# Performance work log

Measured on AMD Instinct MI355X. Metric: run time of the kernel, lower is better.

The kernel has to match this reference:

```python
import jax, jax.numpy as jnp
import numpy as np

TEMPERATURE = 0.1  # init kwarg
EPS = 1e-8        # torch cosine_similarity eps


def setup_inputs() -> dict:
    key = jax.random.key(0)
    k1, k2, k3 = jax.random.split(key, 3)
    B, D, C = 4096, 1024, 32
    representations = jax.random.normal(k1, (B, D), dtype=jnp.float32)
    soft_labels = jax.random.uniform(k2, (B, C), dtype=jnp.float32)
    labels = jax.random.randint(k3, (B,), 0, 32, dtype=jnp.int64)
    return {
        "representations": representations,
        "soft_labels": soft_labels,
        "labels": labels,
        "pseudo_weight": 10,
    }


def reference(representations, soft_labels, labels, pseudo_weight):
    B = representations.shape[0]
    # row-normalize (cosine similarity)
    norms = jnp.maximum(jnp.linalg.norm(representations, axis=1, keepdims=True), EPS)
    rn = representations / norms
    Z = (rn @ rn.T) / TEMPERATURE                      # [B, B] scaled cosine sims
    E = jnp.exp(Z)
    off_diag = 1.0 - jnp.eye(B, dtype=Z.dtype)         # exclude j == i
    denom = jnp.sum(E * off_diag, axis=1, keepdims=True)   # [B, 1]
    loss_arr = -(Z - jnp.log(denom))                   # -log(exp(Z_ij)/denom_i)
    # positive-pair weights: same label, j != i (detached in original)
    pos = (labels[:, None] == labels[None, :]).astype(Z.dtype) * off_diag
    soft_sim = jax.lax.stop_gradient(soft_labels @ soft_labels.T)  # torch.inner, detached
    w = pos + pseudo_weight * soft_sim
    return jnp.sum(loss_arr * w) / B
```

## Files before the change

### kernel.cpp

```cpp
#include <hip/hip_runtime.h>
#include <hip/hip_bf16.h>
#include <stdint.h>


typedef float f32x4 __attribute__((ext_vector_type(4)));
typedef long i64;

#define INV_T 10.0f
#define Z_SCALE (INV_T / 256.0f)

#define GLD16(gp, lp)                                                          \
    __builtin_amdgcn_global_load_lds(                                          \
        (const __attribute__((address_space(1))) uint32_t*)(gp),               \
        (__attribute__((address_space(3))) uint32_t*)(lp), 16, 0, 0)

#define OFF_RNF8  0
#define OFF_DENOM 4194304
#define OFF_POSS  (OFF_DENOM + 16384)
#define OFF_G     (OFF_POSS + 16384)
#define OFF_OACC  (OFF_G + 131072)
#define OFF_DONE  (OFF_OACC + 16)
#define ZERO_SPAN 167936
#define OFF_CSP   (OFF_DENOM + ZERO_SPAN)
#define OFF_CCP   (OFF_CSP + 4096)
#define OFF_W     (OFF_CCP + 4096)

__global__ __launch_bounds__(256) void scl_stage1(const float* __restrict__ rep,
                                                  const float* __restrict__ sl,
                                                  const int* __restrict__ labels,
                                                  uint32_t* __restrict__ rnf8,
                                                  float* __restrict__ cs_part,
                                                  int* __restrict__ cc_part,
                                                  char* __restrict__ zbase) {
    int b = blockIdx.x;
    int t = threadIdx.x;
    if (b < 4096) {
        int row = b;
        const float4* src = reinterpret_cast<const float4*>(rep + (size_t)row * 1024);
        float4 v = src[t];
        float s = v.x * v.x + v.y * v.y + v.z * v.z + v.w * v.w;
#pragma unroll
        for (int m = 1; m < 64; m <<= 1) s += __shfl_xor(s, m, 64);
        __shared__ float red[4];
        if ((t & 63) == 0) red[t >> 6] = s;
        __syncthreads();
        s = red[0] + red[1] + red[2] + red[3];
        float nf = 16.0f / fmaxf(sqrtf(s), 1e-8f);
        int p = 0;
        p = __builtin_amdgcn_cvt_pk_fp8_f32(v.x * nf, v.y * nf, p, false);
        p = __builtin_amdgcn_cvt_pk_fp8_f32(v.z * nf, v.w * nf, p, true);
        rnf8[row * 256 + t] = (uint32_t)p;
    } else if (b < 4128) {
        __shared__ float part[8][32];
        __shared__ int bins[32];
        int bb = b - 4096;
        if (t < 32) bins[t] = 0;
        __syncthreads();
        if (t < 128) atomicAdd(&bins[labels[bb * 128 + t]], 1);
        int c = t & 31, rg = t >> 5;
        float s = 0.f;
#pragma unroll 4
        for (int k = 0; k < 16; ++k) {
            int i = bb * 128 + rg * 16 + k;
            s += sl[i * 32 + c];
        }
        part[rg][c] = s;
        __syncthreads();
        if (t < 32) {
            float tot = 0.f;
#pragma unroll
            for (int g = 0; g < 8; ++g) tot += part[g][t];
            cs_part[bb * 32 + t] = tot;
            cc_part[bb * 32 + t] = bins[t];
        }
    } else {
        int zb = b - 4128;
        *(uint4*)(zbase + (size_t)zb * 4096 + t * 16) = (uint4){0, 0, 0, 0};
    }
}

__global__ __launch_bounds__(256) void scl_main(const uint8_t* __restrict__ rnf8,
                                                const float* __restrict__ sl,
                                                const int* __restrict__ labels,
                                                const float* __restrict__ cs_part,
                                                const int* __restrict__ cc_part,
                                                const int* __restrict__ pwp,
                                                float* __restrict__ denom,
                                                float* __restrict__ posS,
                                                float* __restrict__ G,
                                                float* __restrict__ W) {
    int tid = threadIdx.x;

    if (blockIdx.x >= 528) {
        if (blockIdx.x < 1040) {
            int idx = blockIdx.x - 528;
            int dblk = idx & 15, ks = idx >> 4;
            int dq = tid >> 5, c = tid & 31;
            int d0 = dblk * 64 + dq * 8;
            float acc[8];
#pragma unroll
            for (int j = 0; j < 8; ++j) acc[j] = 0.f;
            int i0 = ks * 128;
#pragma unroll 4
            for (int k = 0; k < 128; ++k) {
                int i = i0 + k;
                uint2 rv = *(const uint2*)&rnf8[(size_t)i * 1024 + d0];
                float sv = sl[i * 32 + c];
                acc[0] += __builtin_amdgcn_cvt_f32_fp8((int)rv.x, 0) * sv;
                acc[1] += __builtin_amdgcn_cvt_f32_fp8((int)rv.x, 1) * sv;
                acc[2] += __builtin_amdgcn_cvt_f32_fp8((int)rv.x, 2) * sv;
                acc[3] += __builtin_amdgcn_cvt_f32_fp8((int)rv.x, 3) * sv;
                acc[4] += __builtin_amdgcn_cvt_f32_fp8((int)rv.y, 0) * sv;
                acc[5] += __builtin_amdgcn_cvt_f32_fp8((int)rv.y, 1) * sv;
                acc[6] += __builtin_amdgcn_cvt_f32_fp8((int)rv.y, 2) * sv;
                acc[7] += __builtin_amdgcn_cvt_f32_fp8((int)rv.y, 3) * sv;
            }
#pragma unroll
            for (int j = 0; j < 8; ++j)
                atomicAdd(&G[(d0 + j) * 32 + c], acc[j] * 0.0625f);
        } else {
            __shared__ __align__(16) float css[32];
            __shared__ int ccs[32];
            if (tid < 32) {
                float s = 0.f; int n = 0;
#pragma unroll
                for (int b = 0; b < 32; ++b) { s += cs_part[b * 32 + tid]; n += cc_part[b * 32 + tid]; }
                css[tid] = s; ccs[tid] = n;
            }
            __syncthreads();
            int bits = *pwp;
            float pw = (bits >= -(1 << 22) && bits <= (1 << 22)) ? (float)bits
                                                                 : __int_as_float(bits);
            int i = (blockIdx.x - 1040) * 256 + tid;
            const f32x4* sl4 = (const f32x4*)sl;
            const f32x4* cs4 = (const f32x4*)css;
            float dW = 0.f;
#pragma unroll
            for (int q = 0; q < 8; ++q) {
                f32x4 s = sl4[i * 8 + q];
                f32x4 c = cs4[q];
                dW += s[0] * c[0] + s[1] * c[1] + s[2] * c[2] + s[3] * c[3];
            }
            W[i] = (float)(ccs[labels[i]] - 1) + pw * dW;
        }
        return;
    }

    __shared__ __align__(16) uint8_t As[2][128 * 64];
    __shared__ __align__(16) uint8_t Bs[2][128 * 64];
    __shared__ int lblA[128], lblB[128];

    int L = blockIdx.x;
    int bi = 0, rem = L;
    while (rem >= 32 - bi) { rem -= 32 - bi; ++bi; }
    int bj = bi + rem;
    int rowA0 = bi * 128, colB0 = bj * 128;

    if (tid < 128) {
        lblA[tid] = labels[rowA0 + tid];
        lblB[tid] = labels[colB0 + tid];
    }

    int lane = tid & 63, warp = tid >> 6;
    int wr = warp >> 1, wc = warp & 1;
    int m_ = lane & 15, g = lane >> 4;

    int r4 = lane >> 2;
    int csw = (lane & 3) ^ ((lane >> 3) & 3);
    const uint8_t* gA0 = rnf8 + (size_t)(rowA0 + warp * 32 + r4) * 1024 + csw * 16;
    const uint8_t* gB0 = rnf8 + (size_t)(colB0 + warp * 32 + r4) * 1024 + csw * 16;

    f32x4 acc[4][4];
#pragma unroll
    for (int a = 0; a < 4; ++a)
#pragma unroll
        for (int b = 0; b < 4; ++b) acc[a][b] = (f32x4){0.f, 0.f, 0.f, 0.f};

    int fsw = (g ^ ((m_ >> 1) & 3)) * 16;

    GLD16(gA0,         &As[0][(warp * 32) * 64]);
    GLD16(gA0 + 16384, &As[0][(warp * 32 + 16) * 64]);
    GLD16(gB0,         &Bs[0][(warp * 32) * 64]);
    GLD16(gB0 + 16384, &Bs[0][(warp * 32 + 16) * 64]);

    for (int kt = 0; kt < 16; ++kt) {
        int cur = kt & 1;
        __syncthreads();
        f32x4 aq[4], bq[4];
#pragma unroll
        for (int ti = 0; ti < 4; ++ti) {
            int rowLoc = wr * 64 + ti * 16 + m_;
            aq[ti] = *(const f32x4*)&As[cur][rowLoc * 64 + fsw];
        }
#pragma unroll
        for (int tj = 0; tj < 4; ++tj) {
            int colLoc = wc * 64 + tj * 16 + m_;
            bq[tj] = *(const f32x4*)&Bs[cur][colLoc * 64 + fsw];
        }
        if (kt < 15) {
            int nxt = cur ^ 1;
            GLD16(gA0 + (kt + 1) * 64,         &As[nxt][(warp * 32) * 64]);
            GLD16(gA0 + (kt + 1) * 64 + 16384, &As[nxt][(warp * 32 + 16) * 64]);
            GLD16(gB0 + (kt + 1) * 64,         &Bs[nxt][(warp * 32) * 64]);
            GLD16(gB0 + (kt + 1) * 64 + 16384, &Bs[nxt][(warp * 32 + 16) * 64]);
        }
#pragma unroll
        for (int s = 0; s < 2; ++s)
#pragma unroll
            for (int ti = 0; ti < 4; ++ti)
#pragma unroll
                for (int tj = 0; tj < 4; ++tj) {
                    i64 a = ((const i64*)&aq[ti])[s];
                    i64 b = ((const i64*)&bq[tj])[s];
                    acc[ti][tj] = __builtin_amdgcn_mfma_f32_16x16x32_fp8_fp8(
                        a, b, acc[ti][tj], 0, 0, 0);
                }
    }

    bool isDiag = (bi == bj);
    int cl = m_;
    float colE[4] = {0.f, 0.f, 0.f, 0.f}, colP[4] = {0.f, 0.f, 0.f, 0.f};
#pragma unroll
    for (int ti = 0; ti < 4; ++ti) {
        int rowLoc = wr * 64 + ti * 16 + g * 4;
        float rE[4] = {0.f, 0.f, 0.f, 0.f}, rP[4] = {0.f, 0.f, 0.f, 0.f};
        int lr[4];
#pragma unroll
        for (int r = 0; r < 4; ++r) lr[r] = lblA[rowLoc + r];
#pragma unroll
        for (int tj = 0; tj < 4; ++tj) {
            int colLoc = wc * 64 + tj * 16 + cl;
            int gCol = colB0 + colLoc;
            int lc = lblB[colLoc];
            f32x4 a = acc[ti][tj];
#pragma unroll
            for (int r = 0; r < 4; ++r) {
                int gRow = rowA0 + rowLoc + r;
                float z = Z_SCALE * a[r];
                float e = __expf(z);
                bool offd = (gRow != gCol);
                if (!offd) e = 0.f;
                rE[r] += e;
                colE[tj] += e;
                if (offd && (lr[r] == lc)) { rP[r] += z; colP[tj] += z; }
            }
        }
#pragma unroll
        for (int r = 0; r < 4; ++r) {
            float v = rE[r], p = rP[r];
#pragma unroll
            for (int msk = 1; msk < 16; msk <<= 1) {
                v += __shfl_xor(v, msk, 64);
                p += __shfl_xor(p, msk, 64);
            }
            if (cl == 0) {
                int gRow = rowA0 + rowLoc + r;
                atomicAdd(&denom[gRow], v);
                atomicAdd(&posS[gRow], p);
            }
        }
    }
    if (!isDiag) {
#pragma unroll
        for (int tj = 0; tj < 4; ++tj) {
            float v = colE[tj], p = colP[tj];
            v += __shfl_xor(v, 16, 64); p += __shfl_xor(p, 16, 64);
            v += __shfl_xor(v, 32, 64); p += __shfl_xor(p, 32, 64);
            if (g == 0) {
                int gCol = colB0 + wc * 64 + tj * 16 + cl;
                atomicAdd(&denom[gCol], v);
                atomicAdd(&posS[gCol], p);
            }
        }
    }
}

__global__ __launch_bounds__(256) void scl_finalize(const float* __restrict__ denom,
                                                    const float* __restrict__ posS,
                                                    const float* __restrict__ W,
                                                    const float* __restrict__ G,
                                                    const int* __restrict__ pwp,
                                                    double* __restrict__ oacc,
                                                    int* __restrict__ done,
                                                    float* __restrict__ out) {
    int t = threadIdx.x;
    __shared__ double wsum[4];
    double contrib = 0.0;

    if (blockIdx.x < 8) {
        int i0 = blockIdx.x * 512 + t;
        float t0 = __logf(denom[i0]) * W[i0] - posS[i0];
        float t1 = __logf(denom[i0 + 256]) * W[i0 + 256] - posS[i0 + 256];
        double td = (double)t0 + (double)t1;
#pragma unroll
        for (int m = 1; m < 64; m <<= 1) td += __shfl_xor(td, m, 64);
        if ((t & 63) == 0) wsum[t >> 6] = td;
        __syncthreads();
        contrib = wsum[0] + wsum[1] + wsum[2] + wsum[3];
    } else {
        int bits = *pwp;
        float pw = (bits >= -(1 << 22) && bits <= (1 << 22)) ? (float)bits
                                                             : __int_as_float(bits);
        const f32x4* G4 = (const f32x4*)G;
        float gs = 0.f;
#pragma unroll
        for (int q = 0; q < 32; ++q) {
            f32x4 v = G4[q * 256 + t];
            gs += v[0] * v[0] + v[1] * v[1] + v[2] * v[2] + v[3] * v[3];
        }
        double gd = (double)gs;
#pragma unroll
        for (int m = 1; m < 64; m <<= 1) gd += __shfl_xor(gd, m, 64);
        if ((t & 63) == 0) wsum[t >> 6] = gd;
        __syncthreads();
        contrib = -(double)(pw * INV_T) * (wsum[0] + wsum[1] + wsum[2] + wsum[3]);
    }

    if (t == 0) {
        atomicAdd(oacc, contrib);
        __threadfence();
        int old = atomicAdd(done, 1);
        if (old == 8) {
            double tot = atomicAdd(oacc, 0.0);
            out[0] = (float)(tot * (1.0 / 4096.0));
        }
    }
}

extern "C" void kernel_launch(void* const* d_in, const int* in_sizes, int n_in,
                              void* d_out, int out_size, void* d_ws, size_t ws_size,
                              hipStream_t stream) {
    const float* rep = (const float*)d_in[0];
    const float* sl = (const float*)d_in[1];
    const int* labels = (const int*)d_in[2];
    const int* pwp = (const int*)d_in[3];

    char* ws = (char*)d_ws;
    uint8_t* rnf8 = (uint8_t*)(ws + OFF_RNF8);
    float* denom = (float*)(ws + OFF_DENOM);
    float* posS = (float*)(ws + OFF_POSS);
    float* G = (float*)(ws + OFF_G);
    double* oacc = (double*)(ws + OFF_OACC);
    int* done = (int*)(ws + OFF_DONE);
    float* cs_part = (float*)(ws + OFF_CSP);
    int* cc_part = (int*)(ws + OFF_CCP);
    float* W = (float*)(ws + OFF_W);

    scl_stage1<<<4169, 256, 0, stream>>>(rep, sl, labels, (uint32_t*)rnf8,
                                         cs_part, cc_part, ws + OFF_DENOM);
    scl_main<<<1056, 256, 0, stream>>>(rnf8, sl, labels, cs_part, cc_part, pwp,
                                       denom, posS, G, W);
    scl_finalize<<<9, 256, 0, stream>>>(denom, posS, W, G, pwp, oacc, done,
                                        (float*)d_out);
}
```

Baseline: 117.5 us.

## Switch symmetric GEMM to 128x64 tiles with interleaved block ordering

The symmetric similarity GEMM now uses 128x64 tiles instead of 128x128, which doubles the GEMM block count (1056) for better load balance across CUs, and shrinks the B LDS buffer and the accumulators. Tile indices are remapped with a strided (bIdx&7)*132 ordering that spreads blocks, likely across XCDs. Column-side reductions are skipped for tiles touching the diagonal 128-row band. The cost is more redundant A-tile loads and more atomics per output.

```diff
diff --git a/kernel.cpp b/kernel.cpp
--- a/kernel.cpp
+++ b/kernel.cpp
@@ -24,6 +24,10 @@
 #define OFF_CSP   (OFF_DENOM + ZERO_SPAN)
 #define OFF_CCP   (OFF_CSP + 4096)
 #define OFF_W     (OFF_CCP + 4096)
+
+#define N_GEMM 1056
+#define N_G    512
+#define N_ALL  (N_GEMM + N_G + 16)
 
 __global__ __launch_bounds__(256) void scl_stage1(const float* __restrict__ rep,
                                                   const float* __restrict__ sl,
@@ -90,10 +94,11 @@
                                                 float* __restrict__ G,
                                                 float* __restrict__ W) {
     int tid = threadIdx.x;
-
-    if (blockIdx.x >= 528) {
-        if (blockIdx.x < 1040) {
-            int idx = blockIdx.x - 528;
+    int bIdx = blockIdx.x;
+
+    if (bIdx >= N_GEMM) {
+        if (bIdx < N_GEMM + N_G) {
+            int idx = bIdx - N_GEMM;
             int dblk = idx & 15, ks = idx >> 4;
             int dq = tid >> 5, c = tid & 31;
             int d0 = dblk * 64 + dq * 8;
@@ -131,7 +136,7 @@
             int bits = *pwp;
             float pw = (bits >= -(1 << 22) && bits <= (1 << 22)) ? (float)bits
                                                                  : __int_as_float(bits);
-            int i = (blockIdx.x - 1040) * 256 + tid;
+            int i = (bIdx - (N_GEMM + N_G)) * 256 + tid;
             const f32x4* sl4 = (const f32x4*)sl;
             const f32x4* cs4 = (const f32x4*)css;
             float dW = 0.f;
@@ -147,19 +152,19 @@
     }
 
     __shared__ __align__(16) uint8_t As[2][128 * 64];
-    __shared__ __align__(16) uint8_t Bs[2][128 * 64];
-    __shared__ int lblA[128], lblB[128];
-
-    int L = blockIdx.x;
+    __shared__ __align__(16) uint8_t Bs[2][64 * 64];
+    __shared__ int lblA[128];
+    __shared__ int lblB[64];
+
+    int L = (bIdx & 7) * 132 + (bIdx >> 3);
     int bi = 0, rem = L;
-    while (rem >= 32 - bi) { rem -= 32 - bi; ++bi; }
-    int bj = bi + rem;
-    int rowA0 = bi * 128, colB0 = bj * 128;
-
-    if (tid < 128) {
-        lblA[tid] = labels[rowA0 + tid];
-        lblB[tid] = labels[colB0 + tid];
-    }
+    while (rem >= 64 - 2 * bi) { rem -= 64 - 2 * bi; ++bi; }
+    int bj = 2 * bi + rem;
+    int rowA0 = bi * 128, colB0 = bj * 64;
+    bool doCol = (bj >= 2 * bi + 2);
+
+    if (tid < 128) lblA[tid] = labels[rowA0 + tid];
+    else if (tid < 192) lblB[tid - 128] = labels[colB0 + (tid - 128)];
 
     int lane = tid & 63, warp = tid >> 6;
     int wr = warp >> 1, wc = warp & 1;
@@ -168,48 +173,46 @@
     int r4 = lane >> 2;
     int csw = (lane & 3) ^ ((lane >> 3) & 3);
     const uint8_t* gA0 = rnf8 + (size_t)(rowA0 + warp * 32 + r4) * 1024 + csw * 16;
-    const uint8_t* gB0 = rnf8 + (size_t)(colB0 + warp * 32 + r4) * 1024 + csw * 16;
-
-    f32x4 acc[4][4];
+    const uint8_t* gB0 = rnf8 + (size_t)(colB0 + warp * 16 + r4) * 1024 + csw * 16;
+
+    f32x4 acc[4][2];
 #pragma unroll
     for (int a = 0; a < 4; ++a)
 #pragma unroll
-        for (int b = 0; b < 4; ++b) acc[a][b] = (f32x4){0.f, 0.f, 0.f, 0.f};
+        for (int b = 0; b < 2; ++b) acc[a][b] = (f32x4){0.f, 0.f, 0.f, 0.f};
 
     int fsw = (g ^ ((m_ >> 1) & 3)) * 16;
 
     GLD16(gA0,         &As[0][(warp * 32) * 64]);
     GLD16(gA0 + 16384, &As[0][(warp * 32 + 16) * 64]);
-    GLD16(gB0,         &Bs[0][(warp * 32) * 64]);
-    GLD16(gB0 + 16384, &Bs[0][(warp * 32 + 16) * 64]);
+    GLD16(gB0,         &Bs[0][(warp * 16) * 64]);
 
     for (int kt = 0; kt < 16; ++kt) {
         int cur = kt & 1;
         __syncthreads();
-        f32x4 aq[4], bq[4];
+        f32x4 aq[4], bq[2];
 #pragma unroll
         for (int ti = 0; ti < 4; ++ti) {
             int rowLoc = wr * 64 + ti * 16 + m_;
             aq[ti] = *(const f32x4*)&As[cur][rowLoc * 64 + fsw];
         }
 #pragma unroll
-        for (int tj = 0; tj < 4; ++tj) {
-            int colLoc = wc * 64 + tj * 16 + m_;
+        for (int tj = 0; tj < 2; ++tj) {
+            int colLoc = wc * 32 + tj * 16 + m_;
             bq[tj] = *(const f32x4*)&Bs[cur][colLoc * 64 + fsw];
         }
         if (kt < 15) {
             int nxt = cur ^ 1;
             GLD16(gA0 + (kt + 1) * 64,         &As[nxt][(warp * 32) * 64]);
             GLD16(gA0 + (kt + 1) * 64 + 16384, &As[nxt][(warp * 32 + 16) * 64]);
-            GLD16(gB0 + (kt + 1) * 64,         &Bs[nxt][(warp * 32) * 64]);
-            GLD16(gB0 + (kt + 1) * 64 + 16384, &Bs[nxt][(warp * 32 + 16) * 64]);
+            GLD16(gB0 + (kt + 1) * 64,         &Bs[nxt][(warp * 16) * 64]);
         }
 #pragma unroll
         for (int s = 0; s < 2; ++s)
 #pragma unroll
             for (int ti = 0; ti < 4; ++ti)
 #pragma unroll
-                for (int tj = 0; tj < 4; ++tj) {
+                for (int tj = 0; tj < 2; ++tj) {
                     i64 a = ((const i64*)&aq[ti])[s];
                     i64 b = ((const i64*)&bq[tj])[s];
                     acc[ti][tj] = __builtin_amdgcn_mfma_f32_16x16x32_fp8_fp8(
@@ -217,9 +220,8 @@
                 }
     }
 
-    bool isDiag = (bi == bj);
     int cl = m_;
-    float colE[4] = {0.f, 0.f, 0.f, 0.f}, colP[4] = {0.f, 0.f, 0.f, 0.f};
+    float colE[2] = {0.f, 0.f}, colP[2] = {0.f, 0.f};
 #pragma unroll
     for (int ti = 0; ti < 4; ++ti) {
         int rowLoc = wr * 64 + ti * 16 + g * 4;
@@ -228,8 +230,8 @@
 #pragma unroll
         for (int r = 0; r < 4; ++r) lr[r] = lblA[rowLoc + r];
 #pragma unroll
-        for (int tj = 0; tj < 4; ++tj) {
-            int colLoc = wc * 64 + tj * 16 + cl;
+        for (int tj = 0; tj < 2; ++tj) {
+            int colLoc = wc * 32 + tj * 16 + cl;
             int gCol = colB0 + colLoc;
             int lc = lblB[colLoc];
             f32x4 a = acc[ti][tj];
@@ -260,14 +262,14 @@
             }
         }
     }
-    if (!isDiag) {
-#pragma unroll
-        for (int tj = 0; tj < 4; ++tj) {
+    if (doCol) {
+#pragma unroll
+        for (int tj = 0; tj < 2; ++tj) {
             float v = colE[tj], p = colP[tj];
             v += __shfl_xor(v, 16, 64); p += __shfl_xor(p, 16, 64);
             v += __shfl_xor(v, 32, 64); p += __shfl_xor(p, 32, 64);
             if (g == 0) {
-                int gCol = colB0 + wc * 64 + tj * 16 + cl;
+                int gCol = colB0 + wc * 32 + tj * 16 + cl;
                 atomicAdd(&denom[gCol], v);
                 atomicAdd(&posS[gCol], p);
             }
@@ -348,8 +350,8 @@
 
     scl_stage1<<<4169, 256, 0, stream>>>(rep, sl, labels, (uint32_t*)rnf8,
                                          cs_part, cc_part, ws + OFF_DENOM);
-    scl_main<<<1056, 256, 0, stream>>>(rnf8, sl, labels, cs_part, cc_part, pwp,
-                                       denom, posS, G, W);
+    scl_main<<<N_ALL, 256, 0, stream>>>(rnf8, sl, labels, cs_part, cc_part, pwp,
+                                        denom, posS, G, W);
     scl_finalize<<<9, 256, 0, stream>>>(denom, posS, W, G, pwp, oacc, done,
                                         (float*)d_out);
 }
```

Result: slower. 126.5 us (+7.7%).

## Triple-buffer fp8 GEMM tiles with prefetch distance two and XCD-aware block remap

Applied to the files above, without the earlier changes.

The Gram-matrix GEMM blocks move from double- to triple-buffered LDS staging. Global-to-LDS loads are now issued two k-steps ahead, with explicit vmcnt waits and raw s_barrier in place of __syncthreads. The intent is to hide more global load latency behind the MFMA work. GEMM tile indices are also remapped with a stride of 66 across groups of 8 blocks, so that consecutive hardware blocks, which likely land on different XCDs, handle neighbouring tiles and share L2 locality. The cost is 50% more LDS per GEMM block, which may reduce occupancy, plus hand-tuned wait counts that depend on the load ordering.

```diff
diff --git a/kernel.cpp b/kernel.cpp
--- a/kernel.cpp
+++ b/kernel.cpp
@@ -24,6 +24,11 @@
 #define OFF_CSP   (OFF_DENOM + ZERO_SPAN)
 #define OFF_CCP   (OFF_CSP + 4096)
 #define OFF_W     (OFF_CCP + 4096)
+
+#define N_GEMM 528
+#define N_G    512
+#define N_W    16
+#define N_ALL  (N_GEMM + N_G + N_W)
 
 __global__ __launch_bounds__(256) void scl_stage1(const float* __restrict__ rep,
                                                   const float* __restrict__ sl,
@@ -90,10 +95,11 @@
                                                 float* __restrict__ G,
                                                 float* __restrict__ W) {
     int tid = threadIdx.x;
-
-    if (blockIdx.x >= 528) {
-        if (blockIdx.x < 1040) {
-            int idx = blockIdx.x - 528;
+    int bIdx = blockIdx.x;
+
+    if (bIdx >= N_GEMM) {
+        if (bIdx < N_GEMM + N_G) {
+            int idx = bIdx - N_GEMM;
             int dblk = idx & 15, ks = idx >> 4;
             int dq = tid >> 5, c = tid & 31;
             int d0 = dblk * 64 + dq * 8;
@@ -131,7 +137,7 @@
             int bits = *pwp;
             float pw = (bits >= -(1 << 22) && bits <= (1 << 22)) ? (float)bits
                                                                  : __int_as_float(bits);
-            int i = (blockIdx.x - 1040) * 256 + tid;
+            int i = (bIdx - (N_GEMM + N_G)) * 256 + tid;
             const f32x4* sl4 = (const f32x4*)sl;
             const f32x4* cs4 = (const f32x4*)css;
             float dW = 0.f;
@@ -146,11 +152,11 @@
         return;
     }
 
-    __shared__ __align__(16) uint8_t As[2][128 * 64];
-    __shared__ __align__(16) uint8_t Bs[2][128 * 64];
+    __shared__ __align__(16) uint8_t As[3][128 * 64];
+    __shared__ __align__(16) uint8_t Bs[3][128 * 64];
     __shared__ int lblA[128], lblB[128];
 
-    int L = blockIdx.x;
+    int L = (bIdx & 7) * 66 + (bIdx >> 3);
     int bi = 0, rem = L;
     while (rem >= 32 - bi) { rem -= 32 - bi; ++bi; }
     int bj = bi + rem;
@@ -178,14 +184,22 @@
 
     int fsw = (g ^ ((m_ >> 1) & 3)) * 16;
 
-    GLD16(gA0,         &As[0][(warp * 32) * 64]);
+    GLD16(gA0,       &As[0][(warp * 32) * 64]);
     GLD16(gA0 + 16384, &As[0][(warp * 32 + 16) * 64]);
-    GLD16(gB0,         &Bs[0][(warp * 32) * 64]);
+    GLD16(gB0,       &Bs[0][(warp * 32) * 64]);
     GLD16(gB0 + 16384, &Bs[0][(warp * 32 + 16) * 64]);
-
-    for (int kt = 0; kt < 16; ++kt) {
-        int cur = kt & 1;
-        __syncthreads();
+    GLD16(gA0 + 64,        &As[1][(warp * 32) * 64]);
+    GLD16(gA0 + 64 + 16384, &As[1][(warp * 32 + 16) * 64]);
+    GLD16(gB0 + 64,        &Bs[1][(warp * 32) * 64]);
+    GLD16(gB0 + 64 + 16384, &Bs[1][(warp * 32 + 16) * 64]);
+
+    asm volatile("s_waitcnt lgkmcnt(0)" ::: "memory");
+
+    for (int kt = 0; kt < 15; ++kt) {
+        int cur = kt % 3;
+        asm volatile("s_waitcnt vmcnt(4)" ::: "memory");
+        __builtin_amdgcn_s_barrier();
+        __builtin_amdgcn_sched_barrier(0);
         f32x4 aq[4], bq[4];
 #pragma unroll
         for (int ti = 0; ti < 4; ++ti) {
@@ -197,12 +211,40 @@
             int colLoc = wc * 64 + tj * 16 + m_;
             bq[tj] = *(const f32x4*)&Bs[cur][colLoc * 64 + fsw];
         }
-        if (kt < 15) {
-            int nxt = cur ^ 1;
-            GLD16(gA0 + (kt + 1) * 64,         &As[nxt][(warp * 32) * 64]);
-            GLD16(gA0 + (kt + 1) * 64 + 16384, &As[nxt][(warp * 32 + 16) * 64]);
-            GLD16(gB0 + (kt + 1) * 64,         &Bs[nxt][(warp * 32) * 64]);
-            GLD16(gB0 + (kt + 1) * 64 + 16384, &Bs[nxt][(warp * 32 + 16) * 64]);
+        if (kt < 14) {
+            int nxt = (kt + 2) % 3;
+            GLD16(gA0 + (kt + 2) * 64,         &As[nxt][(warp * 32) * 64]);
+            GLD16(gA0 + (kt + 2) * 64 + 16384, &As[nxt][(warp * 32 + 16) * 64]);
+            GLD16(gB0 + (kt + 2) * 64,         &Bs[nxt][(warp * 32) * 64]);
+            GLD16(gB0 + (kt + 2) * 64 + 16384, &Bs[nxt][(warp * 32 + 16) * 64]);
+        }
+#pragma unroll
+        for (int s = 0; s < 2; ++s)
+#pragma unroll
+            for (int ti = 0; ti < 4; ++ti)
+#pragma unroll
+                for (int tj = 0; tj < 4; ++tj) {
+                    i64 a = ((const i64*)&aq[ti])[s];
+                    i64 b = ((const i64*)&bq[tj])[s];
+                    acc[ti][tj] = __builtin_amdgcn_mfma_f32_16x16x32_fp8_fp8(
+                        a, b, acc[ti][tj], 0, 0, 0);
+                }
+    }
+    {
+        int cur = 15 % 3;
+        asm volatile("s_waitcnt vmcnt(0)" ::: "memory");
+        __builtin_amdgcn_s_barrier();
+        __builtin_amdgcn_sched_barrier(0);
+        f32x4 aq[4], bq[4];
+#pragma unroll
+        for (int ti = 0; ti < 4; ++ti) {
+            int rowLoc = wr * 64 + ti * 16 + m_;
+            aq[ti] = *(const f32x4*)&As[cur][rowLoc * 64 + fsw];
+        }
+#pragma unroll
+        for (int tj = 0; tj < 4; ++tj) {
+            int colLoc = wc * 64 + tj * 16 + m_;
+            bq[tj] = *(const f32x4*)&Bs[cur][colLoc * 64 + fsw];
         }
 #pragma unroll
         for (int s = 0; s < 2; ++s)
@@ -348,8 +390,8 @@
 
     scl_stage1<<<4169, 256, 0, stream>>>(rep, sl, labels, (uint32_t*)rnf8,
                                          cs_part, cc_part, ws + OFF_DENOM);
-    scl_main<<<1056, 256, 0, stream>>>(rnf8, sl, labels, cs_part, cc_part, pwp,
-                                       denom, posS, G, W);
+    scl_main<<<N_ALL, 256, 0, stream>>>(rnf8, sl, labels, cs_part, cc_part, pwp,
+                                        denom, posS, G, W);
     scl_finalize<<<9, 256, 0, stream>>>(denom, posS, W, G, pwp, oacc, done,
                                         (float*)d_out);
 }
```

Result: no change. 115.9 us (-1.3%).
